# Optimization experiments

Measured on AMD Instinct MI355X. Metric: run time of the kernel, lower is better.

The kernel has to match this reference:

```python
import jax, jax.numpy as jnp
import numpy as np

BN_EPS = 1e-5
CURVE_LENGTH = 8

def _gumbel_st(logits):
    # straight-through gumbel-softmax (no gumbel noise, temperature=1), over last dim
    y = jax.nn.softmax(logits, axis=-1)
    ind = jnp.argmax(y, axis=-1)
    y_hard = jax.nn.one_hot(ind, logits.shape[-1], dtype=y.dtype)
    return jax.lax.stop_gradient(y_hard - y) + y

def _crossover(cur_vec, nb):
    # cur_vec: (B, c), nb: (B, c, k) -> clamp(1 + cosine, 0, 1), detached
    cur_vec = jax.lax.stop_gradient(cur_vec)
    nb = jax.lax.stop_gradient(nb)
    dot = jnp.einsum('bc,bck->bk', cur_vec, nb)
    n1 = jnp.linalg.norm(cur_vec, axis=1, keepdims=True)        # (B, 1)
    n2 = jnp.linalg.norm(nb, axis=1)                            # (B, k)
    cos = dot / jnp.maximum(n1 * n2, 1e-8)
    return jnp.clip(1.0 + cos, 0.0, 1.0)

def walk_forward(x, adj, cur, agent_w, agent_gamma, agent_beta, agent_mean, agent_var,
                 mom_w, mom_gamma, mom_beta, mom_mean, mom_var):
    bn, c, tot = x.shape
    k = adj.shape[-1]
    cn = cur.shape[1]
    flatten_x = jnp.transpose(x, (0, 2, 1)).reshape(bn * tot, c)
    offset = (jnp.arange(bn, dtype=adj.dtype) * tot)[:, None, None]
    tmp_adj = (adj + offset).reshape(bn * tot, k)
    flatten_cur = (cur + offset).reshape(-1)                    # (bn*cn,)
    inv_agent = agent_gamma / jnp.sqrt(agent_var + BN_EPS)      # (1,)
    inv_mom = mom_gamma / jnp.sqrt(mom_var + BN_EPS)            # (2,)
    rows = jnp.arange(bn * cn)
    curves = []
    pre_feature = cur_feature = cur_feature_cos = pre_feature_cos = None
    for step in range(CURVE_LENGTH):
        if step == 0:
            pre_feature = jnp.transpose(flatten_x[flatten_cur].reshape(bn, cn, c, 1), (0, 2, 1, 3))  # (bn,c,cn,1)
        else:
            cat1 = jnp.concatenate([cur_feature[..., 0], pre_feature[..., 0]], axis=1)  # (bn,2c,cn)
            mlog = jnp.einsum('bcn,oc->bon', cat1, mom_w)
            mlog = (mlog - mom_mean[None, :, None]) * inv_mom[None, :, None] + mom_beta[None, :, None]
            att = jax.nn.softmax(mlog, axis=1).reshape(bn, 1, cn, 2)  # faithful to torch .view
            cat2 = jnp.concatenate([cur_feature, pre_feature], axis=-1)  # (bn,c,cn,2)
            pre_feature = jnp.sum(cat2 * att, axis=-1, keepdims=True)    # (bn,c,cn,1)
            pre_feature_cos = jnp.transpose(pre_feature, (0, 2, 1, 3)).reshape(bn * cn, c)
        pick_idx = tmp_adj[flatten_cur]                                  # (bn*cn, k)
        pv_flat = flatten_x[pick_idx.reshape(-1)].reshape(bn * cn, k, c)
        pv_cos = jnp.transpose(pv_flat, (0, 2, 1))                       # (bn*cn, c, k)
        pick_values = jnp.transpose(pv_flat.reshape(bn, cn, k, c), (0, 3, 1, 2))  # (bn,c,cn,k)
        cat3 = jnp.concatenate([pick_values, jnp.broadcast_to(pre_feature, pick_values.shape)], axis=1)  # (bn,2c,cn,k)
        logits = jnp.einsum('bcnk,c->bnk', cat3, agent_w)[:, None]       # conv2d 1x1 -> (bn,1,cn,k)
        logits = (logits - agent_mean[0]) * inv_agent[0] + agent_beta[0]
        if step != 0:
            d = _crossover(cur_feature_cos - pre_feature_cos, pv_cos - cur_feature_cos[..., None])
            logits = logits * d.reshape(bn, cn, k)[:, None]
        sel = _gumbel_st(logits)                                         # (bn,1,cn,k)
        cur_feature = jnp.sum(pick_values * sel, axis=-1, keepdims=True)  # (bn,c,cn,1)
        cur_feature_cos = jnp.transpose(cur_feature, (0, 2, 1, 3)).reshape(bn * cn, c)
        cur_idx = jnp.argmax(sel, axis=-1).reshape(-1)                   # (bn*cn,)
        flatten_cur = pick_idx[rows, cur_idx]
        curves.append(cur_feature)
    return jnp.concatenate(curves, axis=-1)  # (bn, c, cn, curve_length)

def setup_inputs() -> dict:
    key = jax.random.key(0)
    ks = jax.random.split(key, 12)
    bn, c, tot, k, cn = 16, 64, 8192, 20, 512
    xyz = jax.random.normal(ks[0], (bn, 3, tot), dtype=jnp.float32)
    x = jax.random.normal(ks[1], (bn, c, tot), dtype=jnp.float32)
    adj = jax.random.randint(ks[2], (bn, tot, k), 0, tot)
    cur = jax.random.randint(ks[3], (bn, cn, 1), 0, tot)
    sc = 1.0 / np.sqrt(2 * c)
    agent_w = jax.random.normal(ks[4], (2 * c,), dtype=jnp.float32) * sc
    mom_w = jax.random.normal(ks[5], (2, 2 * c), dtype=jnp.float32) * sc
    agent_gamma = 1.0 + 0.1 * jax.random.normal(ks[6], (1,), dtype=jnp.float32)
    agent_beta = 0.1 * jax.random.normal(ks[7], (1,), dtype=jnp.float32)
    agent_mean = 0.1 * jax.random.normal(ks[8], (1,), dtype=jnp.float32)
    agent_var = jax.random.uniform(ks[9], (1,), minval=0.5, maxval=1.5, dtype=jnp.float32)
    mom_gamma = 1.0 + 0.1 * jax.random.normal(ks[10], (2,), dtype=jnp.float32)
    mom_beta = 0.1 * jax.random.normal(ks[11], (2,), dtype=jnp.float32)
    mom_mean = 0.1 * jax.random.normal(jax.random.fold_in(key, 101), (2,), dtype=jnp.float32)
    mom_var = jax.random.uniform(jax.random.fold_in(key, 102), (2,), minval=0.5, maxval=1.5, dtype=jnp.float32)
    return {"xyz": xyz, "x": x, "adj": adj, "cur": cur,
            "agent_w": agent_w, "agent_gamma": agent_gamma, "agent_beta": agent_beta,
            "agent_mean": agent_mean, "agent_var": agent_var,
            "mom_w": mom_w, "mom_gamma": mom_gamma, "mom_beta": mom_beta,
            "mom_mean": mom_mean, "mom_var": mom_var}

def reference(xyz, x, adj, cur, agent_w, agent_gamma, agent_beta, agent_mean, agent_var,
              mom_w, mom_gamma, mom_beta, mom_mean, mom_var):
    # xyz is accepted (as in the torch forward) but never used: the original code
    # calls `xyz.transpose(1, 2).contiguous` without invoking it.
    return walk_forward(x, adj, cur, agent_w, agent_gamma, agent_beta, agent_mean,
                        agent_var, mom_w, mom_gamma, mom_beta, mom_mean, mom_var)
```

## Files before the change

kernel.cpp:

```cpp
#include <hip/hip_runtime.h>
#include <cmath>

#define BN 16
#define CDIM 64
#define TOT 8192
#define KNB 20
#define CN 512
#define NSTEPS 8
#define WPB 16
#define BPB 32
#define WSTRIDE 577
#define POISON 0xAAAAAAAAu

typedef float vf4 __attribute__((ext_vector_type(4)));

__device__ __forceinline__ float dot4(float a, float b, float c, float d,
                                      float wa, float wb, float wc, float wd) {
  return a * wa + b * wb + c * wc + d * wd;
}

template <int CTRL>
__device__ __forceinline__ float dpp_add(float v) {
  int o = __builtin_amdgcn_update_dpp(0, __float_as_int(v), CTRL, 0xF, 0xF, true);
  return v + __int_as_float(o);
}
template <int CTRL>
__device__ __forceinline__ float dppf(float v) {
  return __int_as_float(__builtin_amdgcn_update_dpp(0, __float_as_int(v), CTRL, 0xF, 0xF, true));
}
template <int CTRL>
__device__ __forceinline__ int dppi(int v) {
  return __builtin_amdgcn_update_dpp(0, v, CTRL, 0xF, 0xF, true);
}
template <int MASK>
__device__ __forceinline__ float swzf(float v) {
  return __int_as_float(__builtin_amdgcn_ds_swizzle(__float_as_int(v), MASK));
}
template <int MASK>
__device__ __forceinline__ int swzi(int v) {
  return __builtin_amdgcn_ds_swizzle(v, MASK);
}

__device__ __forceinline__ float gred16(float v) {
  v = dpp_add<0xB1>(v);
  v = dpp_add<0x4E>(v);
  v = dpp_add<0x141>(v);
  v = dpp_add<0x140>(v);
  return v;
}

__device__ __forceinline__ float sred16(float* a, bool L0, bool L1, bool L2, bool L3) {
#pragma unroll
  for (int i = 0; i < 16; ++i) a[i] = a[i] + dppf<0xB1>(a[i]);
  float b[8];
#pragma unroll
  for (int m = 0; m < 8; ++m) b[m] = L0 ? a[2 * m + 1] : a[2 * m];
#pragma unroll
  for (int m = 0; m < 8; ++m) b[m] = b[m] + dppf<0x4E>(b[m]);
  float c[4];
#pragma unroll
  for (int m = 0; m < 4; ++m) c[m] = L1 ? b[2 * m + 1] : b[2 * m];
#pragma unroll
  for (int m = 0; m < 4; ++m) c[m] = c[m] + swzf<0x101F>(c[m]);
  float d[2];
#pragma unroll
  for (int m = 0; m < 2; ++m) d[m] = L2 ? c[2 * m + 1] : c[2 * m];
#pragma unroll
  for (int m = 0; m < 2; ++m) d[m] = d[m] + swzf<0x201F>(d[m]);
  return L3 ? d[1] : d[0];
}

__device__ __forceinline__ float sred4(float* a, bool L0, bool L1) {
#pragma unroll
  for (int i = 0; i < 4; ++i) a[i] = a[i] + dppf<0xB1>(a[i]);
  float b[2];
  b[0] = L0 ? a[1] : a[0];
  b[1] = L0 ? a[3] : a[2];
#pragma unroll
  for (int m = 0; m < 2; ++m) b[m] = b[m] + dppf<0x4E>(b[m]);
  float c = L1 ? b[1] : b[0];
  c = c + swzf<0x101F>(c);
  c = c + swzf<0x201F>(c);
  return c;
}

__device__ __forceinline__ const vf4* vptr(const float* base, unsigned boff) {
  return (const vf4*)((const char*)base + boff);
}
__device__ __forceinline__ float ldf(const float* base, unsigned boff) {
  return *(const float*)((const char*)base + boff);
}

__global__ __launch_bounds__(256) void prep_kernel(
    const float* __restrict__ x, const float* __restrict__ agent_w,
    float* __restrict__ xt, float* __restrict__ pa) {
  __shared__ float tile[64][65];
  const int tid = threadIdx.x;
  const int bI  = blockIdx.x;
  const int b   = (bI & 7) | (((bI >> 10) & 1) << 3);
  const int t0  = ((bI >> 3) & 127) << 6;
  const vf4 awp = *(const vf4*)(agent_w + ((tid & 15) << 2));
  float4 pre[4];
#pragma unroll
  for (int k = 0; k < 4; ++k) {
    int fid = tid + (k << 8);
    int cc = fid >> 4, qt = (fid & 15) << 2;
    pre[k] = *(const float4*)(x + ((size_t)b * CDIM + cc) * TOT + t0 + qt);
  }
#pragma unroll
  for (int k = 0; k < 4; ++k) {
    int fid = tid + (k << 8);
    int cc = fid >> 4, qt = (fid & 15) << 2;
    tile[cc][qt + 0] = pre[k].x; tile[cc][qt + 1] = pre[k].y;
    tile[cc][qt + 2] = pre[k].z; tile[cc][qt + 3] = pre[k].w;
  }
  __syncthreads();
#pragma unroll
  for (int k = 0; k < 4; ++k) {
    int fid = tid + (k << 8);
    int tt = fid >> 4, qc = (fid & 15) << 2;
    vf4 vv = {tile[qc + 0][tt], tile[qc + 1][tt], tile[qc + 2][tt], tile[qc + 3][tt]};
    *(vf4*)(xt + ((size_t)b * TOT + t0 + tt) * CDIM + qc) = vv;
    float part = gred16(dot4(vv.x, vv.y, vv.z, vv.w, awp.x, awp.y, awp.z, awp.w));
    if ((tid & 15) == 0) pa[(size_t)b * TOT + t0 + tt] = part;
  }
}

__global__ __launch_bounds__(256, 2) void walk_kernel(
    const int* __restrict__ adj, const int* __restrict__ cur,
    const float* __restrict__ agent_w, const float* __restrict__ agent_gamma,
    const float* __restrict__ agent_beta, const float* __restrict__ agent_mean,
    const float* __restrict__ agent_var, const float* __restrict__ mom_w,
    const float* __restrict__ mom_gamma, const float* __restrict__ mom_beta,
    const float* __restrict__ mom_mean, const float* __restrict__ mom_var,
    const float* __restrict__ xt, const float* __restrict__ pa,
    float* __restrict__ out, float* __restrict__ sbuf) {
  __shared__ float lds_out[WPB * WSTRIDE];
  const int tid  = threadIdx.x;
  const int lane = tid & 63;
  const int wv   = tid >> 6;
  const int g    = lane >> 4;
  const int L    = lane & 15;
  const bool L0 = L & 1, L1 = L & 2, L2 = L & 4, L3 = L & 8;
  const int b     = (blockIdx.x & 7) + (((blockIdx.x >> 8) & 1) << 3);
  const int chunk = (blockIdx.x >> 3) & 31;
  const int w     = wv * 4 + g;
  const int n     = chunk * WPB + w;
  const int c0    = L << 2;
  const int mbase = (n << 2) & 1023;
  const int moff  = (chunk >= 16) ? 1 : 0;

  const vf4 aw2  = *(const vf4*)(agent_w + 64 + c0);
  const vf4 mw0a = *(const vf4*)(mom_w + c0);
  const vf4 mw0b = *(const vf4*)(mom_w + 64 + c0);
  const vf4 mw1a = *(const vf4*)(mom_w + 128 + c0);
  const vf4 mw1b = *(const vf4*)(mom_w + 192 + c0);
  const float amean  = agent_mean[0];
  const float abeta  = agent_beta[0];
  const float ainv   = agent_gamma[0] / sqrtf(agent_var[0] + 1e-5f);
  const float m0mean = mom_mean[0], m1mean = mom_mean[1];
  const float m0inv  = mom_gamma[0] / sqrtf(mom_var[0] + 1e-5f);
  const float m1inv  = mom_gamma[1] / sqrtf(mom_var[1] + 1e-5f);
  const float m0beta = mom_beta[0], m1beta = mom_beta[1];

  const float* xb   = xt + (size_t)b * TOT * CDIM;
  const float* pab  = pa + (size_t)b * TOT;
  const int*   adjb = adj + (size_t)b * TOT * KNB;
  float*       lout = lds_out + w * WSTRIDE;

  int t = cur[b * CN + n];
  vf4 pf = *vptr(xb, ((unsigned)t << 8) + (unsigned)(c0 << 2));
  vf4 cf = pf;
  vf4 u  = (vf4){0.f, 0.f, 0.f, 0.f};
  float A0v = 0.f, A1v = 0.f;

  vf4   nv[KNB];
  int   tL1, tL2;
  float pvL1, pvL2;
  float sqL1 = 0.f, sqL2 = 0.f;
  {
    const int4* arow = (const int4*)((const char*)adjb + (unsigned)t * 80u);
    int4 q0 = arow[0], q1 = arow[1], q2 = arow[2], q3 = arow[3], q4 = arow[4];
    int tmp[KNB] = {q0.x, q0.y, q0.z, q0.w, q1.x, q1.y, q1.z, q1.w,
                    q2.x, q2.y, q2.z, q2.w, q3.x, q3.y, q3.z, q3.w,
                    q4.x, q4.y, q4.z, q4.w};
#pragma unroll
    for (int j = 0; j < KNB; ++j)
      nv[j] = *vptr(xb, ((unsigned)tmp[j] << 8) + (unsigned)(c0 << 2));
    tL1 = tmp[0];
#pragma unroll
    for (int j = 1; j < 16; ++j) tL1 = (L == j) ? tmp[j] : tL1;
    tL2 = tmp[16];
#pragma unroll
    for (int q = 1; q < 4; ++q) tL2 = ((L & 3) == q) ? tmp[16 + q] : tL2;
    pvL1 = ldf(pab, (unsigned)tL1 << 2) * ainv;
    pvL2 = ldf(pab, (unsigned)tL2 << 2) * ainv;
  }

  __builtin_amdgcn_s_setprio(1);
#pragma unroll 1
  for (int s = 0; s < NSTEPS; ++s) {
    float n1 = 0.f;
    if (s > 0) {
      pf.x = A0v * cf.x + A1v * pf.x;
      pf.y = A0v * cf.y + A1v * pf.y;
      pf.z = A0v * cf.z + A1v * pf.z;
      pf.w = A0v * cf.w + A1v * pf.w;
      u.x = cf.x - pf.x; u.y = cf.y - pf.y; u.z = cf.z - pf.z; u.w = cf.w - pf.w;
      n1 = sqrtf(gred16(u.x * u.x + u.y * u.y + u.z * u.z + u.w * u.w));
    }
    float pw = gred16(pf.x * aw2.x + pf.y * aw2.y + pf.z * aw2.z + pf.w * aw2.w);
    float lbase = (pw - amean) * ainv + abeta;

    float p1, p2;
    if (s > 0) {
      float up[16], up2[4];
#pragma unroll
      for (int j = 0; j < 16; ++j) {
        const vf4 v = nv[j];
        float tx = v.x - cf.x, ty = v.y - cf.y, tz = v.z - cf.z, tw = v.w - cf.w;
        up[j] = tx * u.x + ty * u.y + tz * u.z + tw * u.w;
      }
#pragma unroll
      for (int q = 0; q < 4; ++q) {
        const vf4 v = nv[16 + q];
        float tx = v.x - cf.x, ty = v.y - cf.y, tz = v.z - cf.z, tw = v.w - cf.w;
        up2[q] = tx * u.x + ty * u.y + tz * u.z + tw * u.w;
      }
      float su1 = sred16(up, L0, L1, L2, L3);
      float su2 = sred4(up2, L0, L1);
      float den1  = fmaxf(n1 * sqL1, 1e-8f);
      float cos1  = su1 * __builtin_amdgcn_rcpf(den1);
      float dfac1 = fminf(fmaxf(1.0f + cos1, 0.0f), 1.0f);
      p1 = (pvL1 + lbase) * dfac1;
      float den2  = fmaxf(n1 * sqL2, 1e-8f);
      float cos2  = su2 * __builtin_amdgcn_rcpf(den2);
      float dfac2 = fminf(fmaxf(1.0f + cos2, 0.0f), 1.0f);
      p2 = (pvL2 + lbase) * dfac2;
    } else {
      p1 = pvL1 + lbase;
      p2 = pvL2 + lbase;
    }

    float bp; int bj, bt;
    {
      bool tk = p2 > p1;
      bp = tk ? p2 : p1;
      bj = tk ? (16 + (L & 3)) : L;
      bt = tk ? tL2 : tL1;
    }
#define AMAX_STAGE(GF, GI)                                        \
    {                                                             \
      float po = GF(bp); int jo = GI(bj); int to = GI(bt);        \
      bool better = (po > bp) || ((po == bp) && (jo < bj));       \
      bp = better ? po : bp;                                      \
      bj = better ? jo : bj;                                      \
      bt = better ? to : bt;                                      \
    }
    AMAX_STAGE(dppf<0xB1>, dppi<0xB1>)
    AMAX_STAGE(dppf<0x4E>, dppi<0x4E>)
    AMAX_STAGE(swzf<0x101F>, swzi<0x101F>)
    AMAX_STAGE(swzf<0x201F>, swzi<0x201F>)
#undef AMAX_STAGE

    {
      vf4 bv = nv[0];
#pragma unroll
      for (int j = 1; j < KNB; ++j) {
        bool e = (bj == j);
        bv.x = e ? nv[j].x : bv.x;
        bv.y = e ? nv[j].y : bv.y;
        bv.z = e ? nv[j].z : bv.z;
        bv.w = e ? nv[j].w : bv.w;
      }
      cf = bv;
    }
    t = bt;
    lout[(c0 + 0) * 9 + s] = cf.x;
    lout[(c0 + 1) * 9 + s] = cf.y;
    lout[(c0 + 2) * 9 + s] = cf.z;
    lout[(c0 + 3) * 9 + s] = cf.w;

    if (s < NSTEPS - 1) {
      float p0 = cf.x * mw0a.x + cf.y * mw0a.y + cf.z * mw0a.z + cf.w * mw0a.w +
                 pf.x * mw0b.x + pf.y * mw0b.y + pf.z * mw0b.z + pf.w * mw0b.w;
      float p1m = cf.x * mw1a.x + cf.y * mw1a.y + cf.z * mw1a.z + cf.w * mw1a.w +
                  pf.x * mw1b.x + pf.y * mw1b.y + pf.z * mw1b.z + pf.w * mw1b.w;
      p0  = gred16(p0);
      p1m = gred16(p1m);
      float mlog0 = (p0 - m0mean) * m0inv + m0beta;
      float mlog1 = (p1m - m1mean) * m1inv + m1beta;
      float mx = fmaxf(mlog0, mlog1);
      float e0 = expf(mlog0 - mx), e1 = expf(mlog1 - mx);
      float sinv = 1.0f / (e0 + e1);
      float* sb = sbuf + ((size_t)(b * NSTEPS + s + 1) << 10);
      if (L == 0) {
        unsigned long long pk =
            (unsigned long long)__float_as_uint(e0 * sinv) |
            ((unsigned long long)__float_as_uint(e1 * sinv) << 32);
        __hip_atomic_store((unsigned long long*)sb + n, pk,
                           __ATOMIC_RELAXED, __HIP_MEMORY_SCOPE_AGENT);
      }
      __builtin_amdgcn_s_setprio(0);
      const unsigned* q0p = (const unsigned*)sb + mbase + moff;
      const unsigned* q2p = q0p + 2;
      unsigned w0 = __hip_atomic_load(q0p, __ATOMIC_RELAXED, __HIP_MEMORY_SCOPE_AGENT);
      unsigned w2 = __hip_atomic_load(q2p, __ATOMIC_RELAXED, __HIP_MEMORY_SCOPE_AGENT);
      const int4* arow = (const int4*)((const char*)adjb + (unsigned)t * 80u);
      int4 q0 = arow[0], q1 = arow[1], q2 = arow[2], q3 = arow[3], q4 = arow[4];
      int tmp[KNB] = {q0.x, q0.y, q0.z, q0.w, q1.x, q1.y, q1.z, q1.w,
                      q2.x, q2.y, q2.z, q2.w, q3.x, q3.y, q3.z, q3.w,
                      q4.x, q4.y, q4.z, q4.w};
#pragma unroll
      for (int j = 0; j < KNB; ++j)
        nv[j] = *vptr(xb, ((unsigned)tmp[j] << 8) + (unsigned)(c0 << 2));
      tL1 = tmp[0];
#pragma unroll
      for (int j = 1; j < 16; ++j) tL1 = (L == j) ? tmp[j] : tL1;
      tL2 = tmp[16];
#pragma unroll
      for (int q = 1; q < 4; ++q) tL2 = ((L & 3) == q) ? tmp[16 + q] : tL2;
      pvL1 = ldf(pab, (unsigned)tL1 << 2) * ainv;
      pvL2 = ldf(pab, (unsigned)tL2 << 2) * ainv;
      {
        float sp[16], sp2[4];
#pragma unroll
        for (int j = 0; j < 16; ++j) {
          const vf4 v = nv[j];
          float tx = v.x - cf.x, ty = v.y - cf.y, tz = v.z - cf.z, tw = v.w - cf.w;
          sp[j] = tx * tx + ty * ty + tz * tz + tw * tw;
        }
#pragma unroll
        for (int q2i = 0; q2i < 4; ++q2i) {
          const vf4 v = nv[16 + q2i];
          float tx = v.x - cf.x, ty = v.y - cf.y, tz = v.z - cf.z, tw = v.w - cf.w;
          sp2[q2i] = tx * tx + ty * ty + tz * tz + tw * tw;
        }
        sqL1 = sqrtf(sred16(sp, L0, L1, L2, L3));
        sqL2 = sqrtf(sred4(sp2, L0, L1));
      }
      while (w0 == POISON || w2 == POISON) {
        __builtin_amdgcn_s_sleep(1);
        w0 = __hip_atomic_load(q0p, __ATOMIC_RELAXED, __HIP_MEMORY_SCOPE_AGENT);
        w2 = __hip_atomic_load(q2p, __ATOMIC_RELAXED, __HIP_MEMORY_SCOPE_AGENT);
      }
      A0v = __uint_as_float(w0);
      A1v = __uint_as_float(w2);
      __builtin_amdgcn_s_setprio(1);
      asm volatile("" ::: "memory");
    }
  }

#pragma unroll
  for (int e = 0; e < 4; ++e) {
    const float* src = lout + (c0 + e) * 9;
    float4 w0 = make_float4(src[0], src[1], src[2], src[3]);
    float4 w1 = make_float4(src[4], src[5], src[6], src[7]);
    float* op = out + (((size_t)(b * CDIM + c0 + e) * CN) + n) * NSTEPS;
    *(float4*)(op)     = w0;
    *(float4*)(op + 4) = w1;
  }
}

extern "C" void kernel_launch(void* const* d_in, const int* in_sizes, int n_in,
                              void* d_out, int out_size, void* d_ws, size_t ws_size,
                              hipStream_t stream) {
  (void)in_sizes; (void)n_in; (void)out_size; (void)ws_size;
  const float* x          = (const float*)d_in[1];
  const int*   adj        = (const int*)d_in[2];
  const int*   cur        = (const int*)d_in[3];
  const float* agent_w    = (const float*)d_in[4];
  const float* agent_gamma= (const float*)d_in[5];
  const float* agent_beta = (const float*)d_in[6];
  const float* agent_mean = (const float*)d_in[7];
  const float* agent_var  = (const float*)d_in[8];
  const float* mom_w      = (const float*)d_in[9];
  const float* mom_gamma  = (const float*)d_in[10];
  const float* mom_beta   = (const float*)d_in[11];
  const float* mom_mean   = (const float*)d_in[12];
  const float* mom_var    = (const float*)d_in[13];
  float* out = (float*)d_out;

  char* ws = (char*)d_ws;
  const size_t xt_bytes   = (size_t)BN * TOT * CDIM * sizeof(float);
  const size_t sbuf_bytes = (size_t)BN * NSTEPS * 2 * CN * sizeof(float);
  float* xt   = (float*)ws;
  float* sbuf = (float*)(ws + xt_bytes);
  float* pab  = (float*)(ws + xt_bytes + sbuf_bytes);

  prep_kernel<<<2048, 256, 0, stream>>>(x, agent_w, xt, pab);
  walk_kernel<<<BN * BPB, 256, 0, stream>>>(adj, cur, agent_w, agent_gamma, agent_beta,
                                            agent_mean, agent_var, mom_w, mom_gamma,
                                            mom_beta, mom_mean, mom_var,
                                            xt, pab, out, sbuf);
}
```

Measured before the change: 154.7 us.

## Prefetch neighbor adjacency rows into LDS and precompute momentum dot products

Each lane now loads the adjacency rows of its candidate neighbors from global memory while the current step is still running and stores them in a per-walker LDS table. After the argmax, the next adjacency row comes from LDS, so the dependent global load is removed from the critical path. Per-neighbor momentum dot products are also precomputed and picked with a binary mux tree, which replaces the linear select chain, and thread priority is raised around the argmax. The cost is about 25KB of extra LDS per block, which may hurt occupancy, and 20 extra global row loads per walker per step.

```diff
diff --git a/kernel.cpp b/kernel.cpp
--- a/kernel.cpp
+++ b/kernel.cpp
@@ -84,6 +84,43 @@
   return c;
 }
 
+__device__ __forceinline__ float fmux20(const float* a, int sel) {
+  bool s0 = sel & 1, s1 = sel & 2, s2 = sel & 4, s3 = sel & 8;
+  float p0 = s0 ? a[1]  : a[0],  p1 = s0 ? a[3]  : a[2];
+  float p2 = s0 ? a[5]  : a[4],  p3 = s0 ? a[7]  : a[6];
+  float p4 = s0 ? a[9]  : a[8],  p5 = s0 ? a[11] : a[10];
+  float p6 = s0 ? a[13] : a[12], p7 = s0 ? a[15] : a[14];
+  float q0 = s1 ? p1 : p0, q1 = s1 ? p3 : p2, q2 = s1 ? p5 : p4, q3 = s1 ? p7 : p6;
+  float r0 = s2 ? q1 : q0, r1 = s2 ? q3 : q2;
+  float lo = s3 ? r1 : r0;
+  float h0 = s0 ? a[17] : a[16], h1 = s0 ? a[19] : a[18];
+  float hi = s1 ? h1 : h0;
+  return (sel & 16) ? hi : lo;
+}
+__device__ __forceinline__ vf4 vmux20(const vf4* a, int sel) {
+  bool s0 = sel & 1, s1 = sel & 2, s2 = sel & 4, s3 = sel & 8;
+  vf4 p0 = s0 ? a[1]  : a[0],  p1 = s0 ? a[3]  : a[2];
+  vf4 p2 = s0 ? a[5]  : a[4],  p3 = s0 ? a[7]  : a[6];
+  vf4 p4 = s0 ? a[9]  : a[8],  p5 = s0 ? a[11] : a[10];
+  vf4 p6 = s0 ? a[13] : a[12], p7 = s0 ? a[15] : a[14];
+  vf4 q0 = s1 ? p1 : p0, q1 = s1 ? p3 : p2, q2 = s1 ? p5 : p4, q3 = s1 ? p7 : p6;
+  vf4 r0 = s2 ? q1 : q0, r1 = s2 ? q3 : q2;
+  vf4 lo = s3 ? r1 : r0;
+  vf4 h0 = s0 ? a[17] : a[16], h1 = s0 ? a[19] : a[18];
+  vf4 hi = s1 ? h1 : h0;
+  return (sel & 16) ? hi : lo;
+}
+__device__ __forceinline__ int imux16(const int* a, int sel) {
+  bool s0 = sel & 1, s1 = sel & 2, s2 = sel & 4, s3 = sel & 8;
+  int p0 = s0 ? a[1]  : a[0],  p1 = s0 ? a[3]  : a[2];
+  int p2 = s0 ? a[5]  : a[4],  p3 = s0 ? a[7]  : a[6];
+  int p4 = s0 ? a[9]  : a[8],  p5 = s0 ? a[11] : a[10];
+  int p6 = s0 ? a[13] : a[12], p7 = s0 ? a[15] : a[14];
+  int q0 = s1 ? p1 : p0, q1 = s1 ? p3 : p2, q2 = s1 ? p5 : p4, q3 = s1 ? p7 : p6;
+  int r0 = s2 ? q1 : q0, r1 = s2 ? q3 : q2;
+  return s3 ? r1 : r0;
+}
+
 __device__ __forceinline__ const vf4* vptr(const float* base, unsigned boff) {
   return (const vf4*)((const char*)base + boff);
 }
@@ -136,6 +173,7 @@
     const float* __restrict__ xt, const float* __restrict__ pa,
     float* __restrict__ out, float* __restrict__ sbuf) {
   __shared__ float lds_out[WPB * WSTRIDE];
+  __shared__ int   lds_adj[WPB * KNB * KNB];
   const int tid  = threadIdx.x;
   const int lane = tid & 63;
   const int wv   = tid >> 6;
@@ -167,18 +205,22 @@
   const float* pab  = pa + (size_t)b * TOT;
   const int*   adjb = adj + (size_t)b * TOT * KNB;
   float*       lout = lds_out + w * WSTRIDE;
-
-  int t = cur[b * CN + n];
-  vf4 pf = *vptr(xb, ((unsigned)t << 8) + (unsigned)(c0 << 2));
-  vf4 cf = pf;
+  int*         ladj = lds_adj + w * KNB * KNB;
+
+  vf4 pf, cf;
   vf4 u  = (vf4){0.f, 0.f, 0.f, 0.f};
   float A0v = 0.f, A1v = 0.f;
 
   vf4   nv[KNB];
+  float nvm0[KNB], nvm1[KNB];
   int   tL1, tL2;
   float pvL1, pvL2;
   float sqL1 = 0.f, sqL2 = 0.f;
+
   {
+    int t = cur[b * CN + n];
+    pf = *vptr(xb, ((unsigned)t << 8) + (unsigned)(c0 << 2));
+    cf = pf;
     const int4* arow = (const int4*)((const char*)adjb + (unsigned)t * 80u);
     int4 q0 = arow[0], q1 = arow[1], q2 = arow[2], q3 = arow[3], q4 = arow[4];
     int tmp[KNB] = {q0.x, q0.y, q0.z, q0.w, q1.x, q1.y, q1.z, q1.w,
@@ -187,14 +229,34 @@
 #pragma unroll
     for (int j = 0; j < KNB; ++j)
       nv[j] = *vptr(xb, ((unsigned)tmp[j] << 8) + (unsigned)(c0 << 2));
-    tL1 = tmp[0];
-#pragma unroll
-    for (int j = 1; j < 16; ++j) tL1 = (L == j) ? tmp[j] : tL1;
-    tL2 = tmp[16];
-#pragma unroll
-    for (int q = 1; q < 4; ++q) tL2 = ((L & 3) == q) ? tmp[16 + q] : tL2;
+    tL1 = imux16(tmp, L);
+    {
+      int h0 = L0 ? tmp[17] : tmp[16];
+      int h1 = L0 ? tmp[19] : tmp[18];
+      tL2 = L1 ? h1 : h0;
+    }
     pvL1 = ldf(pab, (unsigned)tL1 << 2) * ainv;
     pvL2 = ldf(pab, (unsigned)tL2 << 2) * ainv;
+#pragma unroll
+    for (int j = 0; j < KNB; ++j) {
+      const vf4 v = nv[j];
+      nvm0[j] = v.x * mw0a.x + v.y * mw0a.y + v.z * mw0a.z + v.w * mw0a.w;
+      nvm1[j] = v.x * mw1a.x + v.y * mw1a.y + v.z * mw1a.z + v.w * mw1a.w;
+    }
+    {
+      const int4* ar = (const int4*)((const char*)adjb + (unsigned)tL1 * 80u);
+      int4 r0 = ar[0], r1 = ar[1], r2 = ar[2], r3 = ar[3], r4 = ar[4];
+      int* dst = ladj + L * KNB;
+      *(int4*)(dst + 0) = r0; *(int4*)(dst + 4) = r1; *(int4*)(dst + 8) = r2;
+      *(int4*)(dst + 12) = r3; *(int4*)(dst + 16) = r4;
+      if (L < 4) {
+        const int4* ar2 = (const int4*)((const char*)adjb + (unsigned)tL2 * 80u);
+        int4 s0 = ar2[0], s1 = ar2[1], s2 = ar2[2], s3 = ar2[3], s4 = ar2[4];
+        int* dst2 = ladj + (16 + L) * KNB;
+        *(int4*)(dst2 + 0) = s0; *(int4*)(dst2 + 4) = s1; *(int4*)(dst2 + 8) = s2;
+        *(int4*)(dst2 + 12) = s3; *(int4*)(dst2 + 16) = s4;
+      }
+    }
   }
 
   __builtin_amdgcn_s_setprio(1);
@@ -242,20 +304,19 @@
       p2 = pvL2 + lbase;
     }
 
-    float bp; int bj, bt;
+    __builtin_amdgcn_s_setprio(3);
+    float bp; int bj;
     {
       bool tk = p2 > p1;
       bp = tk ? p2 : p1;
       bj = tk ? (16 + (L & 3)) : L;
-      bt = tk ? tL2 : tL1;
     }
 #define AMAX_STAGE(GF, GI)                                        \
     {                                                             \
-      float po = GF(bp); int jo = GI(bj); int to = GI(bt);        \
+      float po = GF(bp); int jo = GI(bj);                         \
       bool better = (po > bp) || ((po == bp) && (jo < bj));       \
       bp = better ? po : bp;                                      \
       bj = better ? jo : bj;                                      \
-      bt = better ? to : bt;                                      \
     }
     AMAX_STAGE(dppf<0xB1>, dppi<0xB1>)
     AMAX_STAGE(dppf<0x4E>, dppi<0x4E>)
@@ -263,29 +324,11 @@
     AMAX_STAGE(swzf<0x201F>, swzi<0x201F>)
 #undef AMAX_STAGE
 
-    {
-      vf4 bv = nv[0];
-#pragma unroll
-      for (int j = 1; j < KNB; ++j) {
-        bool e = (bj == j);
-        bv.x = e ? nv[j].x : bv.x;
-        bv.y = e ? nv[j].y : bv.y;
-        bv.z = e ? nv[j].z : bv.z;
-        bv.w = e ? nv[j].w : bv.w;
-      }
-      cf = bv;
-    }
-    t = bt;
-    lout[(c0 + 0) * 9 + s] = cf.x;
-    lout[(c0 + 1) * 9 + s] = cf.y;
-    lout[(c0 + 2) * 9 + s] = cf.z;
-    lout[(c0 + 3) * 9 + s] = cf.w;
-
     if (s < NSTEPS - 1) {
-      float p0 = cf.x * mw0a.x + cf.y * mw0a.y + cf.z * mw0a.z + cf.w * mw0a.w +
-                 pf.x * mw0b.x + pf.y * mw0b.y + pf.z * mw0b.z + pf.w * mw0b.w;
-      float p1m = cf.x * mw1a.x + cf.y * mw1a.y + cf.z * mw1a.z + cf.w * mw1a.w +
-                  pf.x * mw1b.x + pf.y * mw1b.y + pf.z * mw1b.z + pf.w * mw1b.w;
+      float sel0 = fmux20(nvm0, bj);
+      float sel1 = fmux20(nvm1, bj);
+      float p0  = sel0 + pf.x * mw0b.x + pf.y * mw0b.y + pf.z * mw0b.z + pf.w * mw0b.w;
+      float p1m = sel1 + pf.x * mw1b.x + pf.y * mw1b.y + pf.z * mw1b.z + pf.w * mw1b.w;
       p0  = gred16(p0);
       p1m = gred16(p1m);
       float mlog0 = (p0 - m0mean) * m0inv + m0beta;
@@ -302,26 +345,60 @@
                            __ATOMIC_RELAXED, __HIP_MEMORY_SCOPE_AGENT);
       }
       __builtin_amdgcn_s_setprio(0);
+      cf = vmux20(nv, bj);
+      lout[(c0 + 0) * 9 + s] = cf.x;
+      lout[(c0 + 1) * 9 + s] = cf.y;
+      lout[(c0 + 2) * 9 + s] = cf.z;
+      lout[(c0 + 3) * 9 + s] = cf.w;
       const unsigned* q0p = (const unsigned*)sb + mbase + moff;
       const unsigned* q2p = q0p + 2;
       unsigned w0 = __hip_atomic_load(q0p, __ATOMIC_RELAXED, __HIP_MEMORY_SCOPE_AGENT);
       unsigned w2 = __hip_atomic_load(q2p, __ATOMIC_RELAXED, __HIP_MEMORY_SCOPE_AGENT);
-      const int4* arow = (const int4*)((const char*)adjb + (unsigned)t * 80u);
-      int4 q0 = arow[0], q1 = arow[1], q2 = arow[2], q3 = arow[3], q4 = arow[4];
-      int tmp[KNB] = {q0.x, q0.y, q0.z, q0.w, q1.x, q1.y, q1.z, q1.w,
-                      q2.x, q2.y, q2.z, q2.w, q3.x, q3.y, q3.z, q3.w,
-                      q4.x, q4.y, q4.z, q4.w};
+      int tmp[KNB];
+      {
+        const int* src = lds_adj + (w * KNB + bj) * KNB;
+        int4 r0 = *(const int4*)(src + 0);
+        int4 r1 = *(const int4*)(src + 4);
+        int4 r2 = *(const int4*)(src + 8);
+        int4 r3 = *(const int4*)(src + 12);
+        int4 r4 = *(const int4*)(src + 16);
+        tmp[0] = r0.x; tmp[1] = r0.y; tmp[2] = r0.z; tmp[3] = r0.w;
+        tmp[4] = r1.x; tmp[5] = r1.y; tmp[6] = r1.z; tmp[7] = r1.w;
+        tmp[8] = r2.x; tmp[9] = r2.y; tmp[10] = r2.z; tmp[11] = r2.w;
+        tmp[12] = r3.x; tmp[13] = r3.y; tmp[14] = r3.z; tmp[15] = r3.w;
+        tmp[16] = r4.x; tmp[17] = r4.y; tmp[18] = r4.z; tmp[19] = r4.w;
+      }
 #pragma unroll
       for (int j = 0; j < KNB; ++j)
         nv[j] = *vptr(xb, ((unsigned)tmp[j] << 8) + (unsigned)(c0 << 2));
-      tL1 = tmp[0];
-#pragma unroll
-      for (int j = 1; j < 16; ++j) tL1 = (L == j) ? tmp[j] : tL1;
-      tL2 = tmp[16];
-#pragma unroll
-      for (int q = 1; q < 4; ++q) tL2 = ((L & 3) == q) ? tmp[16 + q] : tL2;
+      tL1 = imux16(tmp, L);
+      {
+        int h0 = L0 ? tmp[17] : tmp[16];
+        int h1 = L0 ? tmp[19] : tmp[18];
+        tL2 = L1 ? h1 : h0;
+      }
       pvL1 = ldf(pab, (unsigned)tL1 << 2) * ainv;
       pvL2 = ldf(pab, (unsigned)tL2 << 2) * ainv;
+#pragma unroll
+      for (int j = 0; j < KNB; ++j) {
+        const vf4 v = nv[j];
+        nvm0[j] = v.x * mw0a.x + v.y * mw0a.y + v.z * mw0a.z + v.w * mw0a.w;
+        nvm1[j] = v.x * mw1a.x + v.y * mw1a.y + v.z * mw1a.z + v.w * mw1a.w;
+      }
+      {
+        const int4* ar = (const int4*)((const char*)adjb + (unsigned)tL1 * 80u);
+        int4 r0 = ar[0], r1 = ar[1], r2 = ar[2], r3 = ar[3], r4 = ar[4];
+        int* dst = ladj + L * KNB;
+        *(int4*)(dst + 0) = r0; *(int4*)(dst + 4) = r1; *(int4*)(dst + 8) = r2;
+        *(int4*)(dst + 12) = r3; *(int4*)(dst + 16) = r4;
+        if (L < 4) {
+          const int4* ar2 = (const int4*)((const char*)adjb + (unsigned)tL2 * 80u);
+          int4 s0 = ar2[0], s1 = ar2[1], s2 = ar2[2], s3 = ar2[3], s4 = ar2[4];
+          int* dst2 = ladj + (16 + L) * KNB;
+          *(int4*)(dst2 + 0) = s0; *(int4*)(dst2 + 4) = s1; *(int4*)(dst2 + 8) = s2;
+          *(int4*)(dst2 + 12) = s3; *(int4*)(dst2 + 16) = s4;
+        }
+      }
       {
         float sp[16], sp2[4];
 #pragma unroll
@@ -348,6 +425,13 @@
       A1v = __uint_as_float(w2);
       __builtin_amdgcn_s_setprio(1);
       asm volatile("" ::: "memory");
+    } else {
+      __builtin_amdgcn_s_setprio(0);
+      cf = vmux20(nv, bj);
+      lout[(c0 + 0) * 9 + s] = cf.x;
+      lout[(c0 + 1) * 9 + s] = cf.y;
+      lout[(c0 + 2) * 9 + s] = cf.z;
+      lout[(c0 + 3) * 9 + s] = cf.w;
     }
   }
 
```

Result: slower. 272.4 us (+76.1%).

## Prefetch candidate neighbours' adjacency rows into LDS one step ahead

Applied to the files above, without the earlier changes.

Each lane now loads the adjacency rows of all 20 candidate neighbours right after they are known and stores them in LDS. Once the argmax picks the winner, the next step reads its row from LDS by winner index, so a dependent global load comes off the critical path. The argmax reduction also stops carrying the node index. In exchange each step issues up to 20x more adjacency loads, and the kernel uses about 25 KB more LDS per block, which could hurt occupancy.

```diff
diff --git a/kernel.cpp b/kernel.cpp
--- a/kernel.cpp
+++ b/kernel.cpp
@@ -136,6 +136,7 @@
     const float* __restrict__ xt, const float* __restrict__ pa,
     float* __restrict__ out, float* __restrict__ sbuf) {
   __shared__ float lds_out[WPB * WSTRIDE];
+  __shared__ int   lds_adj[WPB * KNB * KNB];
   const int tid  = threadIdx.x;
   const int lane = tid & 63;
   const int wv   = tid >> 6;
@@ -167,10 +168,9 @@
   const float* pab  = pa + (size_t)b * TOT;
   const int*   adjb = adj + (size_t)b * TOT * KNB;
   float*       lout = lds_out + w * WSTRIDE;
-
-  int t = cur[b * CN + n];
-  vf4 pf = *vptr(xb, ((unsigned)t << 8) + (unsigned)(c0 << 2));
-  vf4 cf = pf;
+  int*         ladj = lds_adj + w * KNB * KNB;
+
+  vf4 pf, cf;
   vf4 u  = (vf4){0.f, 0.f, 0.f, 0.f};
   float A0v = 0.f, A1v = 0.f;
 
@@ -178,7 +178,11 @@
   int   tL1, tL2;
   float pvL1, pvL2;
   float sqL1 = 0.f, sqL2 = 0.f;
+
   {
+    int t = cur[b * CN + n];
+    pf = *vptr(xb, ((unsigned)t << 8) + (unsigned)(c0 << 2));
+    cf = pf;
     const int4* arow = (const int4*)((const char*)adjb + (unsigned)t * 80u);
     int4 q0 = arow[0], q1 = arow[1], q2 = arow[2], q3 = arow[3], q4 = arow[4];
     int tmp[KNB] = {q0.x, q0.y, q0.z, q0.w, q1.x, q1.y, q1.z, q1.w,
@@ -195,6 +199,20 @@
     for (int q = 1; q < 4; ++q) tL2 = ((L & 3) == q) ? tmp[16 + q] : tL2;
     pvL1 = ldf(pab, (unsigned)tL1 << 2) * ainv;
     pvL2 = ldf(pab, (unsigned)tL2 << 2) * ainv;
+    {
+      const int4* ar = (const int4*)((const char*)adjb + (unsigned)tL1 * 80u);
+      int4 r0 = ar[0], r1 = ar[1], r2 = ar[2], r3 = ar[3], r4 = ar[4];
+      int* dst = ladj + L * KNB;
+      *(int4*)(dst + 0) = r0; *(int4*)(dst + 4) = r1; *(int4*)(dst + 8) = r2;
+      *(int4*)(dst + 12) = r3; *(int4*)(dst + 16) = r4;
+      if (L < 4) {
+        const int4* ar2 = (const int4*)((const char*)adjb + (unsigned)tL2 * 80u);
+        int4 s0 = ar2[0], s1 = ar2[1], s2 = ar2[2], s3 = ar2[3], s4 = ar2[4];
+        int* dst2 = ladj + (16 + L) * KNB;
+        *(int4*)(dst2 + 0) = s0; *(int4*)(dst2 + 4) = s1; *(int4*)(dst2 + 8) = s2;
+        *(int4*)(dst2 + 12) = s3; *(int4*)(dst2 + 16) = s4;
+      }
+    }
   }
 
   __builtin_amdgcn_s_setprio(1);
@@ -242,20 +260,18 @@
       p2 = pvL2 + lbase;
     }
 
-    float bp; int bj, bt;
+    float bp; int bj;
     {
       bool tk = p2 > p1;
       bp = tk ? p2 : p1;
       bj = tk ? (16 + (L & 3)) : L;
-      bt = tk ? tL2 : tL1;
     }
 #define AMAX_STAGE(GF, GI)                                        \
     {                                                             \
-      float po = GF(bp); int jo = GI(bj); int to = GI(bt);        \
+      float po = GF(bp); int jo = GI(bj);                         \
       bool better = (po > bp) || ((po == bp) && (jo < bj));       \
       bp = better ? po : bp;                                      \
       bj = better ? jo : bj;                                      \
-      bt = better ? to : bt;                                      \
     }
     AMAX_STAGE(dppf<0xB1>, dppi<0xB1>)
     AMAX_STAGE(dppf<0x4E>, dppi<0x4E>)
@@ -275,7 +291,6 @@
       }
       cf = bv;
     }
-    t = bt;
     lout[(c0 + 0) * 9 + s] = cf.x;
     lout[(c0 + 1) * 9 + s] = cf.y;
     lout[(c0 + 2) * 9 + s] = cf.z;
@@ -306,11 +321,20 @@
       const unsigned* q2p = q0p + 2;
       unsigned w0 = __hip_atomic_load(q0p, __ATOMIC_RELAXED, __HIP_MEMORY_SCOPE_AGENT);
       unsigned w2 = __hip_atomic_load(q2p, __ATOMIC_RELAXED, __HIP_MEMORY_SCOPE_AGENT);
-      const int4* arow = (const int4*)((const char*)adjb + (unsigned)t * 80u);
-      int4 q0 = arow[0], q1 = arow[1], q2 = arow[2], q3 = arow[3], q4 = arow[4];
-      int tmp[KNB] = {q0.x, q0.y, q0.z, q0.w, q1.x, q1.y, q1.z, q1.w,
-                      q2.x, q2.y, q2.z, q2.w, q3.x, q3.y, q3.z, q3.w,
-                      q4.x, q4.y, q4.z, q4.w};
+      int tmp[KNB];
+      {
+        const int* src = ladj + bj * KNB;
+        int4 r0 = *(const int4*)(src + 0);
+        int4 r1 = *(const int4*)(src + 4);
+        int4 r2 = *(const int4*)(src + 8);
+        int4 r3 = *(const int4*)(src + 12);
+        int4 r4 = *(const int4*)(src + 16);
+        tmp[0] = r0.x; tmp[1] = r0.y; tmp[2] = r0.z; tmp[3] = r0.w;
+        tmp[4] = r1.x; tmp[5] = r1.y; tmp[6] = r1.z; tmp[7] = r1.w;
+        tmp[8] = r2.x; tmp[9] = r2.y; tmp[10] = r2.z; tmp[11] = r2.w;
+        tmp[12] = r3.x; tmp[13] = r3.y; tmp[14] = r3.z; tmp[15] = r3.w;
+        tmp[16] = r4.x; tmp[17] = r4.y; tmp[18] = r4.z; tmp[19] = r4.w;
+      }
 #pragma unroll
       for (int j = 0; j < KNB; ++j)
         nv[j] = *vptr(xb, ((unsigned)tmp[j] << 8) + (unsigned)(c0 << 2));
@@ -322,6 +346,20 @@
       for (int q = 1; q < 4; ++q) tL2 = ((L & 3) == q) ? tmp[16 + q] : tL2;
       pvL1 = ldf(pab, (unsigned)tL1 << 2) * ainv;
       pvL2 = ldf(pab, (unsigned)tL2 << 2) * ainv;
+      {
+        const int4* ar = (const int4*)((const char*)adjb + (unsigned)tL1 * 80u);
+        int4 r0 = ar[0], r1 = ar[1], r2 = ar[2], r3 = ar[3], r4 = ar[4];
+        int* dst = ladj + L * KNB;
+        *(int4*)(dst + 0) = r0; *(int4*)(dst + 4) = r1; *(int4*)(dst + 8) = r2;
+        *(int4*)(dst + 12) = r3; *(int4*)(dst + 16) = r4;
+        if (L < 4) {
+          const int4* ar2 = (const int4*)((const char*)adjb + (unsigned)tL2 * 80u);
+          int4 s0 = ar2[0], s1 = ar2[1], s2 = ar2[2], s3 = ar2[3], s4 = ar2[4];
+          int* dst2 = ladj + (16 + L) * KNB;
+          *(int4*)(dst2 + 0) = s0; *(int4*)(dst2 + 4) = s1; *(int4*)(dst2 + 8) = s2;
+          *(int4*)(dst2 + 12) = s3; *(int4*)(dst2 + 16) = s4;
+        }
+      }
       {
         float sp[16], sp2[4];
 #pragma unroll
```

Result: slower. 162.1 us (+4.7%).
